# Kernel optimization log

Measured on AMD Instinct MI355X. Metric: run time of the kernel, lower is better.

Reference implementation:

```python
import jax, jax.numpy as jnp
import numpy as np

N_GRAPHS = 128


def setup_inputs() -> dict:
    key = jax.random.key(0)
    k1, k2, k3, k4, k5, k6, k7 = jax.random.split(key, 7)
    N, E, IN, HID, OUT = 50000, 800000, 64, 64, 2
    x = jax.random.normal(k1, (N, IN), dtype=jnp.float32)
    edge_index = jax.random.randint(k2, (2, E), 0, N, dtype=jnp.int64)
    batch = jnp.sort(jax.random.randint(k3, (N,), 0, N_GRAPHS, dtype=jnp.int64))
    # GCNConv params (glorot-ish) and output Linear params
    W = jax.random.normal(k4, (IN, HID), dtype=jnp.float32) / np.sqrt(IN)
    b = jnp.zeros((HID,), dtype=jnp.float32)
    lin_W = jax.random.normal(k5, (HID, OUT), dtype=jnp.float32) / np.sqrt(HID)
    lin_b = jax.random.normal(k6, (OUT,), dtype=jnp.float32) * 0.01
    return {"x": x, "edge_index": edge_index, "batch": batch,
            "W": W, "b": b, "lin_W": lin_W, "lin_b": lin_b}


def gcn_conv(x, edge_index, W, b):
    N = x.shape[0]
    # add self loops (PyG GCNConv default)
    loop = jnp.arange(N, dtype=edge_index.dtype)
    row = jnp.concatenate([edge_index[0], loop])  # source nodes
    col = jnp.concatenate([edge_index[1], loop])  # target nodes
    # symmetric degree normalization D^{-1/2} (A+I) D^{-1/2}
    deg = jax.ops.segment_sum(jnp.ones_like(col, dtype=x.dtype), col, num_segments=N)
    dinv = jnp.where(deg > 0, jax.lax.rsqrt(jnp.maximum(deg, 1e-12)), 0.0)
    norm = dinv[row] * dinv[col]  # [E+N]
    h = x @ W  # [N, HID] transform before aggregation
    msgs = norm[:, None] * h[row]  # [E+N, HID] gathered messages
    out = jax.ops.segment_sum(msgs, col, num_segments=N)
    return out + b


def reference(x, edge_index, batch, W, b, lin_W, lin_b):
    h = gcn_conv(x, edge_index, W, b)
    h = jax.nn.relu(h)
    # global mean pool over batch ids
    sums = jax.ops.segment_sum(h, batch, num_segments=N_GRAPHS)  # [G, HID]
    cnts = jax.ops.segment_sum(jnp.ones((h.shape[0],), h.dtype), batch, num_segments=N_GRAPHS)
    pooled = sums / jnp.maximum(cnts, 1.0)[:, None]
    # dropout(p=0.2) is identity in eval mode
    return pooled @ lin_W + lin_b  # [G, OUT]
```

## Files before the change

### kernel.cpp

```cpp
#include <hip/hip_runtime.h>
#include <hip/hip_fp16.h>

#define N_NODES 50000
#define N_EDGES 800000
#define FDIM    64
#define NGRAPH  128
#define CAP     64
#define GW      8
#define NPB     32
#define NGSLOT  8
#define NBLK1   200
#define CHUNK_E (N_EDGES / NBLK1)
#define NBKT    196
#define SEGC    64


__global__ void k_bin(const int* __restrict__ row, const int* __restrict__ col,
                      unsigned int* __restrict__ gbin, int* __restrict__ gcnt,
                      float* __restrict__ pooled, float* __restrict__ cnt) {
    __shared__ unsigned int sbuf[NBKT * SEGC];
    __shared__ int scnt[NBKT];
    int tid = threadIdx.x, blk = blockIdx.x;
    if (blk == 0) {
        float4 z = make_float4(0.f, 0.f, 0.f, 0.f);
        float4* p4 = (float4*)pooled;
        for (int i = tid; i < (NGRAPH * FDIM) / 4; i += 256) p4[i] = z;
        float4* c4 = (float4*)cnt;
        if (tid < NGRAPH / 4) c4[tid] = z;
    }
    for (int i = tid; i < NBKT; i += 256) scnt[i] = 0;
    __syncthreads();
    int base = blk * CHUNK_E;
    for (int i = base + tid; i < base + CHUNK_E; i += 256) {
        int c = col[i], r = row[i];
        int s = c >> 8;
        int p = atomicAdd(&scnt[s], 1);
        if (p < SEGC) sbuf[s * SEGC + p] = ((unsigned)(c & 255) << 16) | (unsigned)r;
    }
    __syncthreads();
    const uint4* s4 = (const uint4*)sbuf;
    uint4* g4 = (uint4*)(gbin + (size_t)blk * (NBKT * SEGC));
    for (int i = tid; i < NBKT * SEGC / 4; i += 256) g4[i] = s4[i];
    for (int s = tid; s < NBKT; s += 256) gcnt[s * NBLK1 + blk] = min(scnt[s], SEGC);
}

__global__ void k_commit(const unsigned int* __restrict__ gbin, const int* __restrict__ gcnt,
                         int* __restrict__ fill, unsigned short* __restrict__ ew) {
    __shared__ int cnts[NBLK1];
    __shared__ int fl[256];
    __shared__ unsigned short slots[256 * CAP];
    int b = blockIdx.x, tid = threadIdx.x;
    for (int i = tid; i < NBLK1; i += 256) cnts[i] = gcnt[b * NBLK1 + i];
    fl[tid] = 0;
    __syncthreads();
    for (int idx = tid; idx < NBLK1 * SEGC; idx += 256) {
        int seg = idx >> 6, j = idx & 63;
        if (j < cnts[seg]) {
            unsigned int v = gbin[((size_t)seg * NBKT + b) * SEGC + j];
            int cl = (int)(v >> 16);
            int p = atomicAdd(&fl[cl], 1);
            if (p < CAP) slots[(cl << 6) + p] = (unsigned short)(v & 0xffffu);
        }
    }
    __syncthreads();
    int nd0 = b << 8;
    int nnodes = min(256, N_NODES - nd0);
    uint4* e4 = (uint4*)(ew + ((size_t)nd0 << 6));
    const uint4* s4 = (const uint4*)slots;
    for (int i = tid; i < nnodes * 8; i += 256) e4[i] = s4[i];
    if (tid < nnodes) fill[nd0 + tid] = fl[tid];
}

__global__ void k_gemm_xw(const float* __restrict__ x, const float* __restrict__ W,
                          const int* __restrict__ fill, __half* __restrict__ h2, int n) {
    int f = threadIdx.x & 63;
    int w = threadIdx.x >> 6;
    float Wreg[FDIM];
    #pragma unroll
    for (int k = 0; k < FDIM; ++k) Wreg[k] = W[k * FDIM + f];
    for (int nd = blockIdx.x * 4 + w; nd < n; nd += gridDim.x * 4) {
        const float4* xr4 = (const float4*)(x + (size_t)nd * FDIM);
        float acc = 0.0f;
        #pragma unroll
        for (int k4 = 0; k4 < 16; ++k4) {
            float4 xv = xr4[k4];
            acc = fmaf(xv.x, Wreg[4 * k4],     acc);
            acc = fmaf(xv.y, Wreg[4 * k4 + 1], acc);
            acc = fmaf(xv.z, Wreg[4 * k4 + 2], acc);
            acc = fmaf(xv.w, Wreg[4 * k4 + 3], acc);
        }
        float di = rsqrtf((float)(fill[nd] + 1));
        h2[((size_t)nd << 6) + f] = __float2half(di * acc);
    }
}

#define ACC4(U, AX, AY, AZ, AW)                                        \
    {                                                                  \
        float2 lo_ = __half22float2(*(const __half2*)&(U).x);          \
        float2 hi_ = __half22float2(*(const __half2*)&(U).y);          \
        AX += lo_.x; AY += lo_.y; AZ += hi_.x; AW += hi_.y;            \
    }

__global__ void k_gather_pool(const int* __restrict__ fill, const unsigned short* __restrict__ ew,
                              const uint2* __restrict__ h2q, const float* __restrict__ b,
                              const int* __restrict__ batch,
                              float* __restrict__ pooled, float* __restrict__ cnt) {
    __shared__ float pl[NGSLOT][FDIM];
    __shared__ float pcnt[NGSLOT];
    __shared__ int g_first_s;

    int tid = threadIdx.x;
    int lane    = tid & 63;
    int fp      = lane & 15;
    int quarter = lane >> 4;
    int wv  = tid >> 6;
    int blk0 = blockIdx.x * NPB;

    for (int i = tid; i < NGSLOT * FDIM; i += 256) pl[i >> 6][i & 63] = 0.0f;
    if (tid < NGSLOT) pcnt[tid] = 0.0f;
    if (tid == 0) g_first_s = batch[blk0];
    __syncthreads();
    int g_first = g_first_s;

    int start = blk0 + wv * GW;
    bool active = start < N_NODES;

    if (active) {
        int dg8 = fill[start + (lane & 7)];
        int bt8 = batch[start + (lane & 7)];
        int slots = (int)ew[((size_t)start << 6) + lane];

        float b0 = b[4 * fp], b1 = b[4 * fp + 1], b2 = b[4 * fp + 2], b3 = b[4 * fp + 3];
        float p0 = 0, p1 = 0, p2 = 0, p3 = 0, cacc = 0;
        int gcur = __shfl(bt8, 0);
        #pragma unroll
        for (int i = 0; i < GW; ++i) {
            int nd = start + i;
            int slots_next = (i < GW - 1) ? (int)ew[((size_t)(nd + 1) << 6) + lane] : 0;
            int g = __shfl(bt8, i);
            if (g != gcur) {
                int sl = gcur - g_first;
                if (sl >= 0 && sl < NGSLOT) {
                    if (quarter == 0) {
                        atomicAdd(&pl[sl][4 * fp],     p0);
                        atomicAdd(&pl[sl][4 * fp + 1], p1);
                        atomicAdd(&pl[sl][4 * fp + 2], p2);
                        atomicAdd(&pl[sl][4 * fp + 3], p3);
                    }
                    if (lane == 0) atomicAdd(&pcnt[sl], cacc);
                } else {
                    if (quarter == 0) {
                        atomicAdd(&pooled[gcur * FDIM + 4 * fp],     p0);
                        atomicAdd(&pooled[gcur * FDIM + 4 * fp + 1], p1);
                        atomicAdd(&pooled[gcur * FDIM + 4 * fp + 2], p2);
                        atomicAdd(&pooled[gcur * FDIM + 4 * fp + 3], p3);
                    }
                    if (lane == 0) atomicAdd(&cnt[gcur], cacc);
                }
                p0 = p1 = p2 = p3 = 0; cacc = 0; gcur = g;
            }
            int deg = min(__shfl(dg8, i), CAP);
            float a0x = 0, a0y = 0, a0z = 0, a0w = 0;
            float a1x = 0, a1y = 0, a1z = 0, a1w = 0;
            float a2x = 0, a2y = 0, a2z = 0, a2w = 0;
            float a3x = 0, a3y = 0, a3z = 0, a3w = 0;
            if (quarter == 0) {
                uint2 su = h2q[((size_t)nd << 4) + fp];
                ACC4(su, a0x, a0y, a0z, a0w);
            }
            int e = 0;
            for (; e + 16 <= deg; e += 16) {
                int s0 = __shfl(slots, e + quarter);
                int s1 = __shfl(slots, e + 4 + quarter);
                int s2 = __shfl(slots, e + 8 + quarter);
                int s3 = __shfl(slots, e + 12 + quarter);
                uint2 u0 = h2q[((size_t)s0 << 4) + fp];
                uint2 u1 = h2q[((size_t)s1 << 4) + fp];
                uint2 u2 = h2q[((size_t)s2 << 4) + fp];
                uint2 u3 = h2q[((size_t)s3 << 4) + fp];
                ACC4(u0, a0x, a0y, a0z, a0w);
                ACC4(u1, a1x, a1y, a1z, a1w);
                ACC4(u2, a2x, a2y, a2z, a2w);
                ACC4(u3, a3x, a3y, a3z, a3w);
            }
            for (; e < deg; e += 4) {
                int idx = e + quarter;
                int sx = __shfl(slots, idx < deg ? idx : deg - 1);
                uint2 u = h2q[((size_t)sx << 4) + fp];
                if (idx < deg) ACC4(u, a0x, a0y, a0z, a0w);
            }
            float ax = (a0x + a1x) + (a2x + a3x);
            float ay = (a0y + a1y) + (a2y + a3y);
            float az = (a0z + a1z) + (a2z + a3z);
            float aw = (a0w + a1w) + (a2w + a3w);
            ax += __shfl_xor(ax, 16); ax += __shfl_xor(ax, 32);
            ay += __shfl_xor(ay, 16); ay += __shfl_xor(ay, 32);
            az += __shfl_xor(az, 16); az += __shfl_xor(az, 32);
            aw += __shfl_xor(aw, 16); aw += __shfl_xor(aw, 32);
            float di = rsqrtf((float)(deg + 1));
            p0 += fmaxf(fmaf(di, ax, b0), 0.0f);
            p1 += fmaxf(fmaf(di, ay, b1), 0.0f);
            p2 += fmaxf(fmaf(di, az, b2), 0.0f);
            p3 += fmaxf(fmaf(di, aw, b3), 0.0f);
            cacc += 1.0f;
            slots = slots_next;
        }
        {
            int sl = gcur - g_first;
            if (sl >= 0 && sl < NGSLOT) {
                if (quarter == 0) {
                    atomicAdd(&pl[sl][4 * fp],     p0);
                    atomicAdd(&pl[sl][4 * fp + 1], p1);
                    atomicAdd(&pl[sl][4 * fp + 2], p2);
                    atomicAdd(&pl[sl][4 * fp + 3], p3);
                }
                if (lane == 0) atomicAdd(&pcnt[sl], cacc);
            } else {
                if (quarter == 0) {
                    atomicAdd(&pooled[gcur * FDIM + 4 * fp],     p0);
                    atomicAdd(&pooled[gcur * FDIM + 4 * fp + 1], p1);
                    atomicAdd(&pooled[gcur * FDIM + 4 * fp + 2], p2);
                    atomicAdd(&pooled[gcur * FDIM + 4 * fp + 3], p3);
                }
                if (lane == 0) atomicAdd(&cnt[gcur], cacc);
            }
        }
    }
    __syncthreads();
    for (int idx = tid; idx < NGSLOT * FDIM; idx += 256) {
        int sl = idx >> 6, f = idx & 63;
        float v = pl[sl][f];
        if (v != 0.0f) atomicAdd(&pooled[(g_first + sl) * FDIM + f], v);
    }
    if (tid < NGSLOT) {
        float c = pcnt[tid];
        if (c != 0.0f) atomicAdd(&cnt[g_first + tid], c);
    }
}

__global__ void k_final_lin(const float* __restrict__ pooled, const float* __restrict__ cnt,
                            const float* __restrict__ linW, const float* __restrict__ linb,
                            float* __restrict__ out) {
    int t = threadIdx.x;
    int g = t >> 1;
    int o = t & 1;
    float c = fmaxf(cnt[g], 1.0f);
    float acc = 0.0f;
    #pragma unroll
    for (int k = 0; k < FDIM; ++k) acc = fmaf(pooled[g * FDIM + k], linW[k * 2 + o], acc);
    out[g * 2 + o] = acc / c + linb[o];
}


extern "C" void kernel_launch(void* const* d_in, const int* in_sizes, int n_in,
                              void* d_out, int out_size, void* d_ws, size_t ws_size,
                              hipStream_t stream) {
    const float* x      = (const float*)d_in[0];
    const int*   ei     = (const int*)d_in[1];
    const int*   batch  = (const int*)d_in[2];
    const float* W      = (const float*)d_in[3];
    const float* b      = (const float*)d_in[4];
    const float* linW   = (const float*)d_in[5];
    const float* linb   = (const float*)d_in[6];
    float*       out    = (float*)d_out;

    const int* row = ei;
    const int* col = ei + N_EDGES;

    char* ws = (char*)d_ws;
    size_t off = 0;
    float*          pooled = (float*)         (ws + off); off += (size_t)NGRAPH * FDIM * 4;
    float*          cnt    = (float*)         (ws + off); off += 512;
    int*            fill   = (int*)           (ws + off); off += ((size_t)N_NODES * 4 + 255) / 256 * 256;
    int*            gcnt   = (int*)           (ws + off); off += ((size_t)NBKT * NBLK1 * 4 + 255) / 256 * 256;
    unsigned int*   gbin   = (unsigned int*)  (ws + off); off += (size_t)NBLK1 * NBKT * SEGC * 4;
    unsigned short* ew     = (unsigned short*)(ws + off); off += (size_t)N_NODES * CAP * 2;
    __half*         h2     = (__half*)        (ws + off); off += (size_t)N_NODES * FDIM * 2;

    k_bin<<<NBLK1, 256, 0, stream>>>(row, col, gbin, gcnt, pooled, cnt);

    k_commit<<<NBKT, 256, 0, stream>>>(gbin, gcnt, fill, ew);

    k_gemm_xw<<<1024, 256, 0, stream>>>(x, W, fill, h2, N_NODES);

    int nblocks = (N_NODES + NPB - 1) / NPB;
    k_gather_pool<<<nblocks, 256, 0, stream>>>(fill, ew, (const uint2*)h2, b, batch, pooled, cnt);

    k_final_lin<<<1, 256, 0, stream>>>(pooled, cnt, linW, linb, out);
}
```

Baseline: 97.65 us.

## Fuse bin, commit and GEMM into one cooperative kernel; fold final linear into gather

Merges the binning, commit and x@W stages into one cooperative-launch kernel that separates the phases with grid-wide syncs, so three kernel launches become one. The final linear layer moves into the gather/pool kernel: the last block to finish, found with an atomic ticket counter, computes the output. This removes launch gaps and the tiny final kernel. In exchange it adds grid.sync costs, host-side occupancy and property queries on every launch, and the GEMM phase now runs on at most 768 blocks instead of 1024.

```diff
diff --git a/kernel.cpp b/kernel.cpp
--- a/kernel.cpp
+++ b/kernel.cpp
@@ -1,5 +1,8 @@
 #include <hip/hip_runtime.h>
 #include <hip/hip_fp16.h>
+#include <hip/hip_cooperative_groups.h>
+
+namespace cg = cooperative_groups;
 
 #define N_NODES 50000
 #define N_EDGES 800000
@@ -14,20 +17,23 @@
 #define NBKT    196
 #define SEGC    64
 
-
-__global__ void k_bin(const int* __restrict__ row, const int* __restrict__ col,
-                      unsigned int* __restrict__ gbin, int* __restrict__ gcnt,
-                      float* __restrict__ pooled, float* __restrict__ cnt) {
-    __shared__ unsigned int sbuf[NBKT * SEGC];
-    __shared__ int scnt[NBKT];
-    int tid = threadIdx.x, blk = blockIdx.x;
-    if (blk == 0) {
-        float4 z = make_float4(0.f, 0.f, 0.f, 0.f);
-        float4* p4 = (float4*)pooled;
-        for (int i = tid; i < (NGRAPH * FDIM) / 4; i += 256) p4[i] = z;
-        float4* c4 = (float4*)cnt;
-        if (tid < NGRAPH / 4) c4[tid] = z;
-    }
+struct BinSh { unsigned int sbuf[NBKT * SEGC]; int scnt[NBKT]; };
+struct ComSh { int cnts[NBLK1]; int fl[256]; unsigned short slots[256 * CAP]; };
+union ShU { BinSh bin; ComSh com; };
+
+
+__device__ __forceinline__ void dev_zero(float* pooled, float* cnt, int* done, int tid) {
+    float4 z = make_float4(0.f, 0.f, 0.f, 0.f);
+    float4* p4 = (float4*)pooled;
+    for (int i = tid; i < (NGRAPH * FDIM) / 4; i += 256) p4[i] = z;
+    if (tid < NGRAPH / 4) ((float4*)cnt)[tid] = z;
+    if (tid == 0) *done = 0;
+}
+
+__device__ __forceinline__ void dev_bin(int blk, int tid,
+        const int* __restrict__ row, const int* __restrict__ col,
+        unsigned int* __restrict__ gbin, int* __restrict__ gcnt,
+        unsigned int* sbuf, int* scnt) {
     for (int i = tid; i < NBKT; i += 256) scnt[i] = 0;
     __syncthreads();
     int base = blk * CHUNK_E;
@@ -44,12 +50,10 @@
     for (int s = tid; s < NBKT; s += 256) gcnt[s * NBLK1 + blk] = min(scnt[s], SEGC);
 }
 
-__global__ void k_commit(const unsigned int* __restrict__ gbin, const int* __restrict__ gcnt,
-                         int* __restrict__ fill, unsigned short* __restrict__ ew) {
-    __shared__ int cnts[NBLK1];
-    __shared__ int fl[256];
-    __shared__ unsigned short slots[256 * CAP];
-    int b = blockIdx.x, tid = threadIdx.x;
+__device__ __forceinline__ void dev_commit(int b, int tid,
+        const unsigned int* __restrict__ gbin, const int* __restrict__ gcnt,
+        int* __restrict__ fill, unsigned short* __restrict__ ew,
+        int* cnts, int* fl, unsigned short* slots) {
     for (int i = tid; i < NBLK1; i += 256) cnts[i] = gcnt[b * NBLK1 + i];
     fl[tid] = 0;
     __syncthreads();
@@ -71,14 +75,15 @@
     if (tid < nnodes) fill[nd0 + tid] = fl[tid];
 }
 
-__global__ void k_gemm_xw(const float* __restrict__ x, const float* __restrict__ W,
-                          const int* __restrict__ fill, __half* __restrict__ h2, int n) {
-    int f = threadIdx.x & 63;
-    int w = threadIdx.x >> 6;
+__device__ __forceinline__ void dev_gemm(int tid, int bid, int stride,
+        const float* __restrict__ x, const float* __restrict__ W,
+        const int* __restrict__ fill, __half* __restrict__ h2) {
+    int f = tid & 63;
+    int wv = tid >> 6;
     float Wreg[FDIM];
     #pragma unroll
     for (int k = 0; k < FDIM; ++k) Wreg[k] = W[k * FDIM + f];
-    for (int nd = blockIdx.x * 4 + w; nd < n; nd += gridDim.x * 4) {
+    for (int nd = bid * 4 + wv; nd < N_NODES; nd += stride * 4) {
         const float4* xr4 = (const float4*)(x + (size_t)nd * FDIM);
         float acc = 0.0f;
         #pragma unroll
@@ -94,6 +99,51 @@
     }
 }
 
+__global__ __launch_bounds__(256, 3) void k_build(
+        const int* __restrict__ row, const int* __restrict__ col,
+        unsigned int* __restrict__ gbin, int* __restrict__ gcnt,
+        int* __restrict__ fill, unsigned short* __restrict__ ew,
+        const float* __restrict__ x, const float* __restrict__ W,
+        __half* __restrict__ h2, float* __restrict__ pooled,
+        float* __restrict__ cnt, int* __restrict__ done) {
+    cg::grid_group grid = cg::this_grid();
+    __shared__ ShU sh;
+    int tid = threadIdx.x;
+    if (blockIdx.x == 0) dev_zero(pooled, cnt, done, tid);
+    for (int blk = blockIdx.x; blk < NBLK1; blk += gridDim.x) {
+        dev_bin(blk, tid, row, col, gbin, gcnt, sh.bin.sbuf, sh.bin.scnt);
+        __syncthreads();
+    }
+    grid.sync();
+    for (int b = blockIdx.x; b < NBKT; b += gridDim.x) {
+        dev_commit(b, tid, gbin, gcnt, fill, ew, sh.com.cnts, sh.com.fl, sh.com.slots);
+        __syncthreads();
+    }
+    grid.sync();
+    dev_gemm(tid, blockIdx.x, gridDim.x, x, W, fill, h2);
+}
+
+__global__ void k_bin_f(const int* __restrict__ row, const int* __restrict__ col,
+                        unsigned int* __restrict__ gbin, int* __restrict__ gcnt,
+                        float* __restrict__ pooled, float* __restrict__ cnt,
+                        int* __restrict__ done) {
+    __shared__ BinSh sh;
+    int tid = threadIdx.x;
+    if (blockIdx.x == 0) dev_zero(pooled, cnt, done, tid);
+    dev_bin(blockIdx.x, tid, row, col, gbin, gcnt, sh.sbuf, sh.scnt);
+}
+
+__global__ void k_commit_f(const unsigned int* __restrict__ gbin, const int* __restrict__ gcnt,
+                           int* __restrict__ fill, unsigned short* __restrict__ ew) {
+    __shared__ ComSh sh;
+    dev_commit(blockIdx.x, threadIdx.x, gbin, gcnt, fill, ew, sh.cnts, sh.fl, sh.slots);
+}
+
+__global__ void k_gemm_f(const float* __restrict__ x, const float* __restrict__ W,
+                         const int* __restrict__ fill, __half* __restrict__ h2) {
+    dev_gemm(threadIdx.x, blockIdx.x, gridDim.x, x, W, fill, h2);
+}
+
 #define ACC4(U, AX, AY, AZ, AW)                                        \
     {                                                                  \
         float2 lo_ = __half22float2(*(const __half2*)&(U).x);          \
@@ -104,10 +154,13 @@
 __global__ void k_gather_pool(const int* __restrict__ fill, const unsigned short* __restrict__ ew,
                               const uint2* __restrict__ h2q, const float* __restrict__ b,
                               const int* __restrict__ batch,
-                              float* __restrict__ pooled, float* __restrict__ cnt) {
+                              float* __restrict__ pooled, float* __restrict__ cnt,
+                              const float* __restrict__ linW, const float* __restrict__ linb,
+                              float* __restrict__ out, int* __restrict__ done) {
     __shared__ float pl[NGSLOT][FDIM];
     __shared__ float pcnt[NGSLOT];
     __shared__ int g_first_s;
+    __shared__ int ticket_s;
 
     int tid = threadIdx.x;
     int lane    = tid & 63;
@@ -236,19 +289,24 @@
         float c = pcnt[tid];
         if (c != 0.0f) atomicAdd(&cnt[g_first + tid], c);
     }
-}
-
-__global__ void k_final_lin(const float* __restrict__ pooled, const float* __restrict__ cnt,
-                            const float* __restrict__ linW, const float* __restrict__ linb,
-                            float* __restrict__ out) {
-    int t = threadIdx.x;
-    int g = t >> 1;
-    int o = t & 1;
-    float c = fmaxf(cnt[g], 1.0f);
-    float acc = 0.0f;
-    #pragma unroll
-    for (int k = 0; k < FDIM; ++k) acc = fmaf(pooled[g * FDIM + k], linW[k * 2 + o], acc);
-    out[g * 2 + o] = acc / c + linb[o];
+    __threadfence();
+    __syncthreads();
+    if (tid == 0) ticket_s = atomicAdd(done, 1);
+    __syncthreads();
+    if (ticket_s == (int)gridDim.x - 1) {
+        __threadfence();
+        int g = tid >> 1, o = tid & 1;
+        float c = __hip_atomic_load(&cnt[g], __ATOMIC_RELAXED, __HIP_MEMORY_SCOPE_AGENT);
+        c = fmaxf(c, 1.0f);
+        float acc = 0.0f;
+        #pragma unroll
+        for (int k = 0; k < FDIM; ++k) {
+            float pv = __hip_atomic_load(&pooled[g * FDIM + k], __ATOMIC_RELAXED,
+                                         __HIP_MEMORY_SCOPE_AGENT);
+            acc = fmaf(pv, linW[k * 2 + o], acc);
+        }
+        out[g * 2 + o] = acc / c + linb[o];
+    }
 }
 
 
@@ -271,20 +329,42 @@
     size_t off = 0;
     float*          pooled = (float*)         (ws + off); off += (size_t)NGRAPH * FDIM * 4;
     float*          cnt    = (float*)         (ws + off); off += 512;
+    int*            done   = (int*)           (ws + off); off += 256;
     int*            fill   = (int*)           (ws + off); off += ((size_t)N_NODES * 4 + 255) / 256 * 256;
     int*            gcnt   = (int*)           (ws + off); off += ((size_t)NBKT * NBLK1 * 4 + 255) / 256 * 256;
     unsigned int*   gbin   = (unsigned int*)  (ws + off); off += (size_t)NBLK1 * NBKT * SEGC * 4;
     unsigned short* ew     = (unsigned short*)(ws + off); off += (size_t)N_NODES * CAP * 2;
     __half*         h2     = (__half*)        (ws + off); off += (size_t)N_NODES * FDIM * 2;
 
-    k_bin<<<NBLK1, 256, 0, stream>>>(row, col, gbin, gcnt, pooled, cnt);
-
-    k_commit<<<NBKT, 256, 0, stream>>>(gbin, gcnt, fill, ew);
-
-    k_gemm_xw<<<1024, 256, 0, stream>>>(x, W, fill, h2, N_NODES);
+    int coop_ok = 0;
+    {
+        int maxb = 0;
+        if (hipOccupancyMaxActiveBlocksPerMultiprocessor(&maxb, k_build, 256, 0) == hipSuccess
+            && maxb > 0) {
+            int dev = 0;
+            hipGetDevice(&dev);
+            hipDeviceProp_t prop;
+            if (hipGetDeviceProperties(&prop, dev) == hipSuccess) {
+                int nblk = maxb * prop.multiProcessorCount;
+                if (nblk > 768) nblk = 768;
+                if (nblk >= NBKT) {
+                    void* args[] = {(void*)&row, (void*)&col, (void*)&gbin, (void*)&gcnt,
+                                    (void*)&fill, (void*)&ew, (void*)&x, (void*)&W,
+                                    (void*)&h2, (void*)&pooled, (void*)&cnt, (void*)&done};
+                    if (hipLaunchCooperativeKernel(k_build, dim3(nblk), dim3(256),
+                                                   args, 0, stream) == hipSuccess)
+                        coop_ok = 1;
+                }
+            }
+        }
+    }
+    if (!coop_ok) {
+        k_bin_f<<<NBLK1, 256, 0, stream>>>(row, col, gbin, gcnt, pooled, cnt, done);
+        k_commit_f<<<NBKT, 256, 0, stream>>>(gbin, gcnt, fill, ew);
+        k_gemm_f<<<1024, 256, 0, stream>>>(x, W, fill, h2);
+    }
 
     int nblocks = (N_NODES + NPB - 1) / NPB;
-    k_gather_pool<<<nblocks, 256, 0, stream>>>(fill, ew, (const uint2*)h2, b, batch, pooled, cnt);
-
-    k_final_lin<<<1, 256, 0, stream>>>(pooled, cnt, linW, linb, out);
-}
+    k_gather_pool<<<nblocks, 256, 0, stream>>>(fill, ew, (const uint2*)h2, b, batch,
+                                               pooled, cnt, linW, linb, out, done);
+}
```

Result: slower. 273.6 us (+180.2%).
